# Kernel tuning notes

Hardware: AMD Instinct MI355X
Metric: run time of the kernel (lower is better)

Reference implementation:

```python
import jax, jax.numpy as jnp
import numpy as np

# WGS84 constants
_A = 6378137.0
_E2 = 6.69437999014e-3  # first eccentricity squared

ALPHA = 1.0
GAMMA = 2.0
DYNAMIC_GAMMA = True
SCALE_FACTOR = 1.0


def _geodetic_to_ecef(lat_rad, lon_rad, h):
    sl, cl = jnp.sin(lat_rad), jnp.cos(lat_rad)
    so, co = jnp.sin(lon_rad), jnp.cos(lon_rad)
    N = _A / jnp.sqrt(1.0 - _E2 * sl * sl)
    x = (N + h) * cl * co
    y = (N + h) * cl * so
    z = (N * (1.0 - _E2) + h) * sl
    return jnp.stack([x, y, z], axis=-1)


def setup_inputs() -> dict:
    key = jax.random.key(0)
    k1, k2, k3, k4 = jax.random.split(key, 4)
    B = 4_000_000
    lat = jax.random.uniform(k1, (B,), jnp.float32, -80.0, 80.0)    # degrees
    lon = jax.random.uniform(k2, (B,), jnp.float32, -180.0, 180.0)  # degrees
    h = jax.random.uniform(k3, (B,), jnp.float32, 0.0, 1000.0)      # meters
    targets = jnp.stack([lat, lon, h], axis=1)
    ref_ecef = _geodetic_to_ecef(jnp.deg2rad(lat), jnp.deg2rad(lon), h)
    # predicted ECEF = true ECEF + ~meters of noise -> realistic GNSS error
    inputs = ref_ecef + 2.0 * jax.random.normal(k4, (B, 3), jnp.float32)
    return {"inputs": inputs, "targets": targets}


def _ecef_to_enu(pred_ecef, gt_geodetic):
    # Batched version of the per-sample ecef_to_enu_torch loop.
    lat = jnp.deg2rad(gt_geodetic[:, 0])
    lon = jnp.deg2rad(gt_geodetic[:, 1])
    h = gt_geodetic[:, 2]
    ref = _geodetic_to_ecef(lat, lon, h)
    d = pred_ecef - ref  # [B,3]
    sl, cl = jnp.sin(lat), jnp.cos(lat)
    so, co = jnp.sin(lon), jnp.cos(lon)
    dx, dy, dz = d[:, 0], d[:, 1], d[:, 2]
    e = -so * dx + co * dy
    n = -sl * co * dx - sl * so * dy + cl * dz
    u = cl * co * dx + cl * so * dy + sl * dz
    return jnp.stack([e, n, u], axis=1)  # [B,3]


def reference(inputs, targets):
    enu_errors = _ecef_to_enu(inputs, targets)                 # [B,3]
    squared_dist = jnp.sqrt(jnp.sum(enu_errors * enu_errors, axis=1))  # L2 norm [B]
    base_loss = squared_dist
    if DYNAMIC_GAMMA:
        dyn_gamma = GAMMA * jnp.exp(-SCALE_FACTOR * base_loss)
    else:
        dyn_gamma = GAMMA
    focal_weight = jnp.power(1.0 - jnp.sqrt(squared_dist / (jnp.max(squared_dist) + 1e-8)), dyn_gamma)
    focal_loss = ALPHA * focal_weight * base_loss
    return jnp.sqrt(jnp.mean(focal_loss * focal_loss))
```

## Files before the change

### kernel.cpp

```cpp
#include <hip/hip_runtime.h>
#include <hip/hip_fp16.h>
#include <math.h>


#define THREADS 256
#define PART_CAP 8192
#define BMAX_OFF 64
#define PART_OFF (64 + PART_CAP * 4)
#define DIST_OFF (1 << 20)

__device__ __forceinline__ void sincos8(const double* __restrict__ x,
                                        double* __restrict__ s,
                                        double* __restrict__ c) {
    const double TWO_OVER_PI = 0.636619772367581343076;
    const double PIO2_HI = 1.57079632679489655800e+00;
    const double PIO2_LO = 6.12323399573676603587e-17;

    double kd[8], r[8], r2[8];
    int q[8];
#pragma unroll
    for (int j = 0; j < 8; ++j) {
        kd[j] = rint(x[j] * TWO_OVER_PI);
        q[j] = ((int)kd[j]) & 3;
    }
#pragma unroll
    for (int j = 0; j < 8; ++j) {
        double rr = fma(-kd[j], PIO2_HI, x[j]);
        r[j] = fma(-kd[j], PIO2_LO, rr);
        r2[j] = r[j] * r[j];
    }
    double ps[8], pc[8];
#pragma unroll
    for (int j = 0; j < 8; ++j) { ps[j] = -2.50507602534068634195e-08;
                                  pc[j] =  2.08757232129817482790e-09; }
#pragma unroll
    for (int j = 0; j < 8; ++j) { ps[j] = fma(ps[j], r2[j],  2.75573137070700676789e-06);
                                  pc[j] = fma(pc[j], r2[j], -2.75573143513906633035e-07); }
#pragma unroll
    for (int j = 0; j < 8; ++j) { ps[j] = fma(ps[j], r2[j], -1.98412698298579493134e-04);
                                  pc[j] = fma(pc[j], r2[j],  2.48015872894767294178e-05); }
#pragma unroll
    for (int j = 0; j < 8; ++j) { ps[j] = fma(ps[j], r2[j],  8.33333333332248946124e-03);
                                  pc[j] = fma(pc[j], r2[j], -1.38888888888741095749e-03); }
#pragma unroll
    for (int j = 0; j < 8; ++j) { ps[j] = fma(ps[j], r2[j], -1.66666666666666324348e-01);
                                  pc[j] = fma(pc[j], r2[j],  4.16666666666666019037e-02); }
#pragma unroll
    for (int j = 0; j < 8; ++j) {
        double sv = fma(r2[j] * r[j], ps[j], r[j]);
        double cv = fma(r2[j] * r2[j], pc[j], fma(-0.5, r2[j], 1.0));
        double sr = (q[j] & 1) ? cv : sv;
        double cr = (q[j] & 1) ? sv : cv;
        s[j] = (q[j] & 2) ? -sr : sr;
        c[j] = ((q[j] + 1) & 2) ? -cr : cr;
    }
}

__device__ __forceinline__ void dist_group4(const float* __restrict__ lat,
                                            const float* __restrict__ lon,
                                            const float* __restrict__ hh,
                                            const float* __restrict__ px,
                                            const float* __restrict__ py,
                                            const float* __restrict__ pz,
                                            float* __restrict__ dout) {
    const float D2R = (float)0.017453292519943295;
    double x[8], s8[8], c8[8];
#pragma unroll
    for (int j = 0; j < 4; ++j) x[j] = (double)(lat[j] * D2R);
#pragma unroll
    for (int j = 0; j < 4; ++j) x[4 + j] = (double)(lon[j] * D2R);
    sincos8(x, s8, c8);

    const double A = 6378137.0, E2 = 0.00669437999014;
#pragma unroll
    for (int j = 0; j < 4; ++j) {
        double sl = s8[j], cl = c8[j], so = s8[4 + j], co = c8[4 + j];
        double h = (double)hh[j];
        double w = fma(-E2 * sl, sl, 1.0);
        double y = fma(-0.5, w, 1.5);
        y = y * fma(-0.5 * w, y * y, 1.5);
        y = y * fma(-0.5 * w, y * y, 1.5);
        double N = A * y, Nh = N + h;
        double X = Nh * cl * co;
        double Y = Nh * cl * so;
        double Z = fma(N, -E2, N + h) * sl;
        double dx = (double)px[j] - X;
        double dy = (double)py[j] - Y;
        double dz = (double)pz[j] - Z;
        dout[j] = sqrtf((float)(dx * dx + dy * dy + dz * dz));
    }
}

__device__ __forceinline__ float dist_one(float latd, float lond, float hf,
                                          float pxx, float pyy, float pzz) {
    float lat[4] = {latd, latd, latd, latd}, lon[4] = {lond, lond, lond, lond};
    float hh[4] = {hf, hf, hf, hf};
    float px[4] = {pxx, pxx, pxx, pxx}, py[4] = {pyy, pyy, pyy, pyy}, pz[4] = {pzz, pzz, pzz, pzz};
    float d[4];
    dist_group4(lat, lon, hh, px, py, pz, d);
    return d[0];
}

#define UNPACK4(ta, tb, tc, lat, lon, hh)                         \
    float lat[4] = {ta.x, ta.w, tb.z, tc.y};                      \
    float lon[4] = {ta.y, tb.x, tb.w, tc.z};                      \
    float hh[4]  = {ta.z, tb.y, tc.x, tc.w};

__device__ __forceinline__ void store_half4(__half* p, float d0, float d1, float d2, float d3) {
    union { __half2 h2[2]; uint2 u; } pk;
    pk.h2[0] = __floats2half2_rn(d0, d1);
    pk.h2[1] = __floats2half2_rn(d2, d3);
    *(uint2*)p = pk.u;
}

__global__ __launch_bounds__(THREADS, 3)
void k_pass1(const float* __restrict__ inp, const float* __restrict__ tgt,
             __half* __restrict__ dist_arr, float* __restrict__ blockmax, long B) {
    long ngroups = (B + 3) >> 2;
    long nthreads = (long)gridDim.x * blockDim.x;
    long gstride = 2 * nthreads;
    float lmax = 0.0f;
    for (long g = (long)blockIdx.x * blockDim.x + threadIdx.x; g < ngroups; g += gstride) {
        long gA = g;
        long gB = g + nthreads;
        long baseA = gA << 2;
        long baseB = gB << 2;
        bool fastA = (baseA + 3 < B);
        bool fastB = (gB < ngroups) && (baseB + 3 < B);

        if (fastA && fastB) {
            const float4* tA = (const float4*)(tgt + 3 * baseA);
            const float4* pA = (const float4*)(inp + 3 * baseA);
            const float4* tB = (const float4*)(tgt + 3 * baseB);
            const float4* pB = (const float4*)(inp + 3 * baseB);
            float4 ta0 = tA[0], ta1 = tA[1], ta2 = tA[2];
            float4 pa0 = pA[0], pa1 = pA[1], pa2 = pA[2];
            float4 tb0 = tB[0], tb1 = tB[1], tb2 = tB[2];
            float4 pb0 = pB[0], pb1 = pB[1], pb2 = pB[2];

            UNPACK4(ta0, ta1, ta2, latA, lonA, hhA);
            UNPACK4(pa0, pa1, pa2, pxA, pyA, pzA);
            float dA[4];
            dist_group4(latA, lonA, hhA, pxA, pyA, pzA, dA);

            UNPACK4(tb0, tb1, tb2, latB, lonB, hhB);
            UNPACK4(pb0, pb1, pb2, pxB, pyB, pzB);
            float dB[4];
            dist_group4(latB, lonB, hhB, pxB, pyB, pzB, dB);

            if (dist_arr) {
                store_half4(dist_arr + baseA, dA[0], dA[1], dA[2], dA[3]);
                store_half4(dist_arr + baseB, dB[0], dB[1], dB[2], dB[3]);
            }
            lmax = fmaxf(lmax, fmaxf(fmaxf(dA[0], dA[1]), fmaxf(dA[2], dA[3])));
            lmax = fmaxf(lmax, fmaxf(fmaxf(dB[0], dB[1]), fmaxf(dB[2], dB[3])));
        } else {
            for (int pass = 0; pass < 2; ++pass) {
                long gg = pass ? gB : gA;
                if (gg >= ngroups) continue;
                long base = gg << 2;
                long end = base + 4 < B ? base + 4 : B;
                for (long i = base; i < end; ++i) {
                    float d = dist_one(tgt[3*i], tgt[3*i+1], tgt[3*i+2],
                                       inp[3*i], inp[3*i+1], inp[3*i+2]);
                    if (dist_arr) dist_arr[i] = __float2half_rn(d);
                    lmax = fmaxf(lmax, d);
                }
            }
        }
    }
    for (int off = 32; off > 0; off >>= 1)
        lmax = fmaxf(lmax, __shfl_down(lmax, off, 64));
    __shared__ float smax[THREADS / 64];
    if ((threadIdx.x & 63) == 0) smax[threadIdx.x >> 6] = lmax;
    __syncthreads();
    if (threadIdx.x == 0) {
        float m = smax[0];
        for (int w = 1; w < THREADS / 64; ++w) m = fmaxf(m, smax[w]);
        blockmax[blockIdx.x] = m;
    }
}

__device__ __forceinline__ double focal2(float d, float denom) {
    float g = 2.0f * __expf(-d);
    float b = 1.0f - sqrtf(d / denom);
    b = fmaxf(b, 0.0f);
    float wgt = __builtin_amdgcn_exp2f(g * __log2f(b));
    float fl = wgt * d;
    return (double)fl * (double)fl;
}

__global__ void k_pass2(const __half* __restrict__ dist_arr,
                        const float* __restrict__ inp,
                        const float* __restrict__ tgt,
                        const float* __restrict__ blockmax, int nb1,
                        double* __restrict__ partials, long B) {
    __shared__ float smax[THREADS / 64];
    __shared__ double sacc[THREADS / 64];
    __shared__ float sb;
    int tid = threadIdx.x;

    float m = 0.0f;
    for (int i = tid; i < nb1; i += THREADS) m = fmaxf(m, blockmax[i]);
    for (int off = 32; off > 0; off >>= 1)
        m = fmaxf(m, __shfl_down(m, off, 64));
    if ((tid & 63) == 0) smax[tid >> 6] = m;
    __syncthreads();
    if (tid == 0) {
        float mm = smax[0];
        for (int w = 1; w < THREADS / 64; ++w) mm = fmaxf(mm, smax[w]);
        sb = mm;
    }
    __syncthreads();
    float denom = sb + 1e-8f;

    long ngroups = (B + 3) >> 2;
    long gstride = (long)gridDim.x * blockDim.x;
    double acc = 0.0;
    for (long g = (long)blockIdx.x * blockDim.x + tid; g < ngroups; g += gstride) {
        long base = g << 2;
        if (base + 3 < B) {
            float d0, d1, d2, d3;
            if (dist_arr) {
                union { uint2 u; __half2 h2[2]; } pk;
                pk.u = *(const uint2*)(dist_arr + base);
                float2 lo = __half22float2(pk.h2[0]);
                float2 hi = __half22float2(pk.h2[1]);
                d0 = lo.x; d1 = lo.y; d2 = hi.x; d3 = hi.y;
            } else {
                const float4* t4 = (const float4*)(tgt + 3 * base);
                float4 ta = t4[0], tb = t4[1], tc = t4[2];
                const float4* p4 = (const float4*)(inp + 3 * base);
                float4 pa = p4[0], pb = p4[1], pc = p4[2];
                UNPACK4(ta, tb, tc, lat, lon, hh);
                UNPACK4(pa, pb, pc, px, py, pz);
                float d[4];
                dist_group4(lat, lon, hh, px, py, pz, d);
                d0 = d[0]; d1 = d[1]; d2 = d[2]; d3 = d[3];
            }
            acc += focal2(d0, denom) + focal2(d1, denom)
                 + focal2(d2, denom) + focal2(d3, denom);
        } else {
            for (long i = base; i < B; ++i) {
                float d = dist_arr ? __half2float(dist_arr[i])
                                   : dist_one(tgt[3*i], tgt[3*i+1], tgt[3*i+2],
                                              inp[3*i], inp[3*i+1], inp[3*i+2]);
                acc += focal2(d, denom);
            }
        }
    }
    for (int off = 32; off > 0; off >>= 1)
        acc += __shfl_down(acc, off, 64);
    if ((tid & 63) == 0) sacc[tid >> 6] = acc;
    __syncthreads();
    if (tid == 0) {
        double s = sacc[0];
        for (int w = 1; w < THREADS / 64; ++w) s += sacc[w];
        partials[blockIdx.x] = s;
    }
}

__global__ void k_final(const double* __restrict__ partials, int nparts,
                        float* __restrict__ out, long B) {
    double acc = 0.0;
    for (int i = threadIdx.x; i < nparts; i += blockDim.x) acc += partials[i];
    for (int off = 32; off > 0; off >>= 1)
        acc += __shfl_down(acc, off, 64);
    __shared__ double lds[THREADS / 64];
    if ((threadIdx.x & 63) == 0) lds[threadIdx.x >> 6] = acc;
    __syncthreads();
    if (threadIdx.x == 0) {
        double s = lds[0];
        for (int w = 1; w < THREADS / 64; ++w) s += lds[w];
        out[0] = (float)sqrt(s / (double)B);
    }
}

extern "C" void kernel_launch(void* const* d_in, const int* in_sizes, int n_in,
                              void* d_out, int out_size, void* d_ws, size_t ws_size,
                              hipStream_t stream) {
    const float* inp = (const float*)d_in[0];
    const float* tgt = (const float*)d_in[1];
    float* out = (float*)d_out;
    long B = (long)in_sizes[0] / 3;

    float* blockmax = (float*)((char*)d_ws + BMAX_OFF);
    double* partials = (double*)((char*)d_ws + PART_OFF);
    __half* dist_arr = nullptr;
    size_t need = (size_t)DIST_OFF + (size_t)B * sizeof(__half);
    if (ws_size >= need) dist_arr = (__half*)((char*)d_ws + DIST_OFF);

    long ngroups = (B + 3) >> 2;

    long nhalf = (ngroups + 1) >> 1;
    int nb1 = (int)((nhalf + THREADS - 1) / THREADS);
    if (nb1 > PART_CAP) nb1 = PART_CAP;
    if (nb1 < 1) nb1 = 1;

    int nb2 = (int)((ngroups + THREADS - 1) / THREADS);
    if (nb2 > PART_CAP) nb2 = PART_CAP;
    if (nb2 < 1) nb2 = 1;

    k_pass1<<<nb1, THREADS, 0, stream>>>(inp, tgt, dist_arr, blockmax, B);
    k_pass2<<<nb2, THREADS, 0, stream>>>(dist_arr, inp, tgt, blockmax, nb1, partials, B);
    k_final<<<1, THREADS, 0, stream>>>(partials, nb2, out, B);
}
```

Baseline: 130.5 us.

## Fuse distance, focal and final reductions into one cooperative kernel

```diff
diff --git a/kernel.cpp b/kernel.cpp
--- a/kernel.cpp
+++ b/kernel.cpp
@@ -1,13 +1,18 @@
 #include <hip/hip_runtime.h>
+#include <hip/hip_cooperative_groups.h>
 #include <hip/hip_fp16.h>
 #include <math.h>
 
 
 #define THREADS 256
+#define MAXG 8
+#define NBMAX 512
 #define PART_CAP 8192
 #define BMAX_OFF 64
 #define PART_OFF (64 + PART_CAP * 4)
 #define DIST_OFF (1 << 20)
+
+namespace cg = cooperative_groups;
 
 __device__ __forceinline__ void sincos8(const double* __restrict__ x,
                                         double* __restrict__ s,
@@ -105,6 +110,120 @@
     float lat[4] = {ta.x, ta.w, tb.z, tc.y};                      \
     float lon[4] = {ta.y, tb.x, tb.w, tc.z};                      \
     float hh[4]  = {ta.z, tb.y, tc.x, tc.w};
+
+__device__ __forceinline__ double focal2(float d, float denom) {
+    float g = 2.0f * __expf(-d);
+    float b = 1.0f - sqrtf(d / denom);
+    b = fmaxf(b, 0.0f);
+    float wgt = __builtin_amdgcn_exp2f(g * __log2f(b));
+    float fl = wgt * d;
+    return (double)fl * (double)fl;
+}
+
+__global__ __launch_bounds__(THREADS, 2)
+void k_fused(const float* __restrict__ inp, const float* __restrict__ tgt,
+             float* __restrict__ blockmax, double* __restrict__ partials,
+             float* __restrict__ out, int nb, long B) {
+    __shared__ float sdist[MAXG * THREADS * 4];
+    __shared__ float smax[THREADS / 64];
+    __shared__ double sacc[THREADS / 64];
+    __shared__ float sden;
+
+    cg::grid_group grid = cg::this_grid();
+    int tid = threadIdx.x;
+    long ngroups = (B + 3) >> 2;
+    long gstride = (long)nb * THREADS;
+
+    float lmax = 0.0f;
+    int k = 0;
+    for (long g = (long)blockIdx.x * THREADS + tid; g < ngroups; g += gstride, ++k) {
+        long base = g << 2;
+        float d[4];
+        if (base + 3 < B) {
+            const float4* t4 = (const float4*)(tgt + 3 * base);
+            float4 ta = t4[0], tb = t4[1], tc = t4[2];
+            const float4* p4 = (const float4*)(inp + 3 * base);
+            float4 pa = p4[0], pb = p4[1], pc = p4[2];
+            UNPACK4(ta, tb, tc, lat, lon, hh);
+            UNPACK4(pa, pb, pc, px, py, pz);
+            dist_group4(lat, lon, hh, px, py, pz, d);
+        } else {
+            for (int j = 0; j < 4; ++j) {
+                long i = base + j;
+                d[j] = (i < B) ? dist_one(tgt[3*i], tgt[3*i+1], tgt[3*i+2],
+                                          inp[3*i], inp[3*i+1], inp[3*i+2])
+                               : 0.0f;
+            }
+        }
+        *(float4*)(sdist + (k * THREADS + tid) * 4) = make_float4(d[0], d[1], d[2], d[3]);
+        lmax = fmaxf(lmax, fmaxf(fmaxf(d[0], d[1]), fmaxf(d[2], d[3])));
+    }
+    for (int off = 32; off > 0; off >>= 1)
+        lmax = fmaxf(lmax, __shfl_down(lmax, off, 64));
+    if ((tid & 63) == 0) smax[tid >> 6] = lmax;
+    __syncthreads();
+    if (tid == 0) {
+        float m = smax[0];
+        for (int w = 1; w < THREADS / 64; ++w) m = fmaxf(m, smax[w]);
+        blockmax[blockIdx.x] = m;
+    }
+
+    grid.sync();
+
+    float m = 0.0f;
+    for (int i = tid; i < nb; i += THREADS) m = fmaxf(m, blockmax[i]);
+    for (int off = 32; off > 0; off >>= 1)
+        m = fmaxf(m, __shfl_down(m, off, 64));
+    if ((tid & 63) == 0) smax[tid >> 6] = m;
+    __syncthreads();
+    if (tid == 0) {
+        float mm = smax[0];
+        for (int w = 1; w < THREADS / 64; ++w) mm = fmaxf(mm, smax[w]);
+        sden = mm + 1e-8f;
+    }
+    __syncthreads();
+    float denom = sden;
+
+    double acc = 0.0;
+    int k2 = 0;
+    for (long g = (long)blockIdx.x * THREADS + tid; g < ngroups; g += gstride, ++k2) {
+        long base = g << 2;
+        float4 dv = *(const float4*)(sdist + (k2 * THREADS + tid) * 4);
+        if (base + 3 < B) {
+            acc += focal2(dv.x, denom) + focal2(dv.y, denom)
+                 + focal2(dv.z, denom) + focal2(dv.w, denom);
+        } else {
+            float dd[4] = {dv.x, dv.y, dv.z, dv.w};
+            for (int j = 0; j < 4; ++j)
+                if (base + j < B) acc += focal2(dd[j], denom);
+        }
+    }
+    for (int off = 32; off > 0; off >>= 1)
+        acc += __shfl_down(acc, off, 64);
+    if ((tid & 63) == 0) sacc[tid >> 6] = acc;
+    __syncthreads();
+    if (tid == 0) {
+        double s = sacc[0];
+        for (int w = 1; w < THREADS / 64; ++w) s += sacc[w];
+        partials[blockIdx.x] = s;
+    }
+
+    grid.sync();
+
+    if (blockIdx.x == 0) {
+        double a2 = 0.0;
+        for (int i = tid; i < nb; i += THREADS) a2 += partials[i];
+        for (int off = 32; off > 0; off >>= 1)
+            a2 += __shfl_down(a2, off, 64);
+        if ((tid & 63) == 0) sacc[tid >> 6] = a2;
+        __syncthreads();
+        if (tid == 0) {
+            double s = sacc[0];
+            for (int w = 1; w < THREADS / 64; ++w) s += sacc[w];
+            out[0] = (float)sqrt(s / (double)B);
+        }
+    }
+}
 
 __device__ __forceinline__ void store_half4(__half* p, float d0, float d1, float d2, float d3) {
     union { __half2 h2[2]; uint2 u; } pk;
@@ -179,15 +298,6 @@
         for (int w = 1; w < THREADS / 64; ++w) m = fmaxf(m, smax[w]);
         blockmax[blockIdx.x] = m;
     }
-}
-
-__device__ __forceinline__ double focal2(float d, float denom) {
-    float g = 2.0f * __expf(-d);
-    float b = 1.0f - sqrtf(d / denom);
-    b = fmaxf(b, 0.0f);
-    float wgt = __builtin_amdgcn_exp2f(g * __log2f(b));
-    float fl = wgt * d;
-    return (double)fl * (double)fl;
 }
 
 __global__ void k_pass2(const __half* __restrict__ dist_arr,
@@ -286,11 +396,23 @@
 
     float* blockmax = (float*)((char*)d_ws + BMAX_OFF);
     double* partials = (double*)((char*)d_ws + PART_OFF);
+
+    long ngroups = (B + 3) >> 2;
+
+    long nbl = (ngroups + (long)THREADS * MAXG - 1) / ((long)THREADS * MAXG);
+    if (nbl < 1) nbl = 1;
+    if (nbl <= NBMAX) {
+        int nb = (int)nbl;
+        void* args[] = { (void*)&inp, (void*)&tgt, (void*)&blockmax,
+                         (void*)&partials, (void*)&out, (void*)&nb, (void*)&B };
+        hipLaunchCooperativeKernel((const void*)k_fused, dim3(nb), dim3(THREADS),
+                                   args, 0, stream);
+        return;
+    }
+
     __half* dist_arr = nullptr;
     size_t need = (size_t)DIST_OFF + (size_t)B * sizeof(__half);
     if (ws_size >= need) dist_arr = (__half*)((char*)d_ws + DIST_OFF);
-
-    long ngroups = (B + 3) >> 2;
 
     long nhalf = (ngroups + 1) >> 1;
     int nb1 = (int)((nhalf + THREADS - 1) / THREADS);
```

Result: slower. 225.8 us (+73.1%).
